# Kernel optimization log

Hardware: AMD Instinct MI355X
Metric: run time of the kernel (lower is better)

Reference implementation:

```python
import jax, jax.numpy as jnp
from jax import lax
import numpy as np

B, T, H, W = 32, 16, 64, 64
LAT, HID, NL = 256, 256, 10
CH = 32  # c_hid
DN = ('NCHW', 'OIHW', 'NCHW')


def setup_inputs() -> dict:
    key = jax.random.key(0)
    keys = iter(jax.random.split(key, 64))
    def rn(shape, scale=0.05):
        return jax.random.normal(next(keys), shape, jnp.float32) * scale
    inp = {}
    inp['x'] = jax.random.normal(next(keys), (B, T, H, W), jnp.float32)
    inp['t'] = jax.random.normal(next(keys), (B, T, H, W), jnp.float32)
    # encoder convs (torch Conv2d weight layout: (out,in,kh,kw))
    inp['ec1_w'] = rn((CH, 1, 3, 3));        inp['ec1_b'] = rn((CH,))
    inp['ec2_w'] = rn((CH, CH, 3, 3));       inp['ec2_b'] = rn((CH,))
    inp['ec3_w'] = rn((2*CH, CH, 3, 3));     inp['ec3_b'] = rn((2*CH,))
    inp['ec4_w'] = rn((2*CH, 2*CH, 3, 3));   inp['ec4_b'] = rn((2*CH,))
    inp['ec5_w'] = rn((2*CH, 2*CH, 3, 3));   inp['ec5_b'] = rn((2*CH,))
    inp['el_w'] = rn((LAT, 2*CH*8*8));       inp['el_b'] = rn((LAT,))
    # decoder (ConvTranspose2d weight layout: (in,out,kh,kw))
    inp['dl_w'] = rn((2*CH*8*8, LAT));       inp['dl_b'] = rn((2*CH*8*8,))
    inp['dt1_w'] = rn((2*CH, 2*CH, 3, 3));   inp['dt1_b'] = rn((2*CH,))
    inp['dc1_w'] = rn((2*CH, 2*CH, 3, 3));   inp['dc1_b'] = rn((2*CH,))
    inp['dt2_w'] = rn((2*CH, CH, 3, 3));     inp['dt2_b'] = rn((CH,))
    inp['dc2_w'] = rn((CH, CH, 3, 3));       inp['dc2_b'] = rn((CH,))
    inp['dt3_w'] = rn((CH, 1, 3, 3));        inp['dt3_b'] = rn((1,))
    # 10 stacked LSTMCells (LAT == HID so layer 0 weight shape matches the rest)
    inp['Wih'] = rn((NL, 4*HID, HID))
    inp['Whh'] = rn((NL, 4*HID, HID))
    inp['bih'] = rn((NL, 4*HID))
    inp['bhh'] = rn((NL, 4*HID))
    inp['lw'] = rn((LAT, HID));  inp['lb'] = rn((LAT,))
    return inp


def gelu(v):
    return jax.nn.gelu(v, approximate=False)


def conv(x, w, b, stride):
    y = lax.conv_general_dilated(x, w, (stride, stride), [(1, 1), (1, 1)], dimension_numbers=DN)
    return y + b[None, :, None, None]


def tconv(x, w, b):
    # torch ConvTranspose2d(k=3, stride=2, padding=1, output_padding=1):
    # flip kernel, swap in/out channels, lhs_dilation=2, pad (lo=1, hi=2)
    wf = jnp.transpose(w[:, :, ::-1, ::-1], (1, 0, 2, 3))
    y = lax.conv_general_dilated(x, wf, (1, 1), [(1, 2), (1, 2)], lhs_dilation=(2, 2), dimension_numbers=DN)
    return y + b[None, :, None, None]


def reference(x, t, ec1_w, ec1_b, ec2_w, ec2_b, ec3_w, ec3_b, ec4_w, ec4_b, ec5_w, ec5_b,
              el_w, el_b, dl_w, dl_b, dt1_w, dt1_b, dc1_w, dc1_b, dt2_w, dt2_b,
              dc2_w, dc2_b, dt3_w, dt3_b, Wih, Whh, bih, bhh, lw, lb):

    def encode(imgs):                              # (N,1,64,64) -> (N,LAT)
        h = gelu(conv(imgs, ec1_w, ec1_b, 2))      # 32x32
        h = gelu(conv(h, ec2_w, ec2_b, 1))
        h = gelu(conv(h, ec3_w, ec3_b, 2))         # 16x16
        h = gelu(conv(h, ec4_w, ec4_b, 1))
        h = gelu(conv(h, ec5_w, ec5_b, 2))         # 8x8
        return h.reshape(h.shape[0], -1) @ el_w.T + el_b

    def decode(z):                                 # (N,LAT) -> (N,1,64,64)
        h = gelu(z @ dl_w.T + dl_b).reshape(z.shape[0], 2*CH, 8, 8)
        h = gelu(tconv(h, dt1_w, dt1_b))           # 16x16
        h = gelu(conv(h, dc1_w, dc1_b, 1))
        h = gelu(tconv(h, dt2_w, dt2_b))           # 32x32
        h = gelu(conv(h, dc2_w, dc2_b, 1))
        return jnp.tanh(tconv(h, dt3_w, dt3_b))    # 64x64

    def cell_stack(h, c, xin):                     # h,c: (NL,B,HID)
        hs, cs = [], []
        prev = xin
        for l in range(NL):
            z = prev @ Wih[l].T + bih[l] + h[l] @ Whh[l].T + bhh[l]
            i, f, g, o = jnp.split(z, 4, axis=-1)
            cl = jax.nn.sigmoid(f) * c[l] + jax.nn.sigmoid(i) * jnp.tanh(g)
            hl = jax.nn.sigmoid(o) * jnp.tanh(cl)
            hs.append(hl); cs.append(cl); prev = hl
        out = prev @ lw.T + lb                     # skip=False
        return jnp.stack(hs), jnp.stack(cs), out

    f_x_t = jnp.concatenate((x, t), axis=1)        # (B,2T,H,W)
    z_x_t = encode(f_x_t.reshape(-1, 1, H, W)).reshape(B, 2 * T, LAT)
    z_x = z_x_t[:, :T]

    h0 = jnp.zeros((NL, B, HID), x.dtype)
    c0 = jnp.zeros((NL, B, HID), x.dtype)

    def step1(carry, xin):
        h, c = carry
        h, c, out = cell_stack(h, c, xin)
        return (h, c), out

    (hT, cT), outs1 = lax.scan(step1, (h0, c0), jnp.swapaxes(z_x, 0, 1))

    def step2(carry, _):
        h, c, xin = carry
        h, c, out = cell_stack(h, c, xin)
        return (h, c, out), out

    _, outs2 = lax.scan(step2, (hT, cT, outs1[-1]), None, length=T)

    outputs = jnp.swapaxes(jnp.concatenate((outs1, outs2), axis=0), 0, 1)  # (B,2T,LAT)
    y_t = outputs[:, T - 1:-1]                    # (B,T,LAT)

    f_t_ = decode(y_t.reshape(B * T, LAT))        # (B*T,1,H,W)
    loss_pred = jnp.mean((f_t_ - f_x_t[:, T:].reshape(-1, 1, H, W)) ** 2)

    f_x_ = decode(z_x.reshape(B * T, LAT))        # rec_loss=True branch
    loss_rec = jnp.mean((f_x_ - f_x_t[:, :T].reshape(-1, 1, H, W)) ** 2)

    return loss_pred, loss_rec, f_t_.reshape(B, T, H, W)
```

## Files before the change

### kernel.cpp

```cpp
#include <hip/hip_runtime.h>
#include <math.h>

#define DEV __device__ __forceinline__

typedef __attribute__((ext_vector_type(8))) short bf8_t;
typedef __attribute__((ext_vector_type(4))) float f4_t;
typedef unsigned short us;

DEV float sigm_f(float v) { return 1.0f / (1.0f + __expf(-v)); }
DEV float tanh_f(float v) { return fmaf(-2.0f, 1.0f / (1.0f + __expf(2.0f * v)), 1.0f); }
DEV float gelu_f(float v) {
  float u = 0.79788456080f * fmaf(0.044715f * v * v, v, v);
  return 0.5f * v * (1.0f + tanh_f(u));
}
DEV unsigned short f2bf(float f) {
  unsigned u = __float_as_uint(f);
  u = (u + 0x7FFFu + ((u >> 16) & 1u)) >> 16;
  return (unsigned short)u;
}
DEV void astore(unsigned* p, unsigned v) {
  __hip_atomic_store(p, v, __ATOMIC_RELAXED, __HIP_MEMORY_SCOPE_AGENT);
}

DEV void prep_norm(int li, const float* w, us* wb, int CIN) {
// ... 22 lines not shown
    const float* __restrict__ dt2, const float* __restrict__ dc2,
    us* __restrict__ o_ec2, us* __restrict__ o_ec3,
    us* __restrict__ o_ec4, us* __restrict__ o_ec5,
    us* __restrict__ o_dt1, us* __restrict__ o_dc1,
    us* __restrict__ o_dt2, us* __restrict__ o_dc2,
    const float* __restrict__ Wih, const float* __restrict__ lw,
    const float* __restrict__ lb,  const float* __restrict__ bih,
    us* __restrict__ wih0b, us* __restrict__ lwTb,
    us* __restrict__ lwbp,  float* __restrict__ beff,
    const float* __restrict__ el_w, const float* __restrict__ dl_w,
    us* __restrict__ elWb, us* __restrict__ dlWb)
{
  int idx = blockIdx.x * 256 + threadIdx.x;
  if (idx < 202752) {
    if (idx < 9216)        prep_norm(idx,          ec2, o_ec2, 32);
    else if (idx < 27648)  prep_norm(idx - 9216,   ec3, o_ec3, 32);
    else if (idx < 64512)  prep_norm(idx - 27648,  ec4, o_ec4, 64);
    else if (idx < 101376) prep_norm(idx - 64512,  ec5, o_ec5, 64);
    else if (idx < 138240) prep_par (idx - 101376, dt1, o_dt1, 64, 64);
    else if (idx < 175104) prep_norm(idx - 138240, dc1, o_dc1, 64);
    else if (idx < 193536) prep_par (idx - 175104, dt2, o_dt2, 32, 64);
    else                   prep_norm(idx - 193536, dc2, o_dc2, 32);
  } else if (idx < 596992) {
    int i2 = idx - 202752;
    if (i2 < 262144) {
      wih0b[i2] = f2bf(Wih[i2]);
    } else if (i2 < 327680) {
      int i = i2 - 262144;
      int n = i & 255, kcol = i >> 8;
      lwTb[i] = f2bf(lw[(size_t)n * 256 + kcol]);
    } else if (i2 < 393216) {
      int i = i2 - 327680;
      lwbp[i] = f2bf(lw[i]);
    } else if (i2 < 394240) {
      int j = i2 - 393216;
      float s = bih[j];
      const float* row = Wih + (size_t)j * 256;
      for (int n = 0; n < 256; ++n) s = fmaf(row[n], lb[n], s);
      beff[j] = s;
    }
  } else {
    int i3 = idx - 596992;
    if (i3 < 1048576) {
      int kn = i3 & 4095, n = i3 >> 12;
      elWb[i3] = f2bf(el_w[(size_t)n * 4096 + ((kn & 63) * 64 + (kn >> 6))]);
    } else {
      int i = i3 - 1048576;
      int k = i & 255, nout = i >> 8;
      dlWb[i] = f2bf(dl_w[(size_t)((nout & 63) * 64 + (nout >> 6)) * 256 + k]);
    }
  }
}

__global__ __launch_bounds__(256) void prep_wl1_k(
    const us* __restrict__ src, us* __restrict__ wb)
{
  int idx = blockIdx.x * 256 + threadIdx.x;
  int e = idx & 7, lane = (idx >> 3) & 63, ks = (idx >> 9) & 7, nt = idx >> 12;
  wb[idx] = src[(size_t)(nt * 16 + (lane & 15)) * 256 + ks * 32 + (lane >> 4) * 8 + e];
}

__global__ __launch_bounds__(256) void ec1_k(
    const float* __restrict__ x,
    const float* __restrict__ w, const float* __restrict__ bias,
    us* __restrict__ out)
{
  __shared__ float sw[288];
  __shared__ float sb[32];
  for (int i = threadIdx.x; i < 288; i += 256) sw[i] = w[i];
  if (threadIdx.x < 32) sb[threadIdx.x] = bias[threadIdx.x];
  __syncthreads();
  int idx = blockIdx.x * 256 + threadIdx.x;
  int ox = idx & 31, oy = (idx >> 5) & 31, n = idx >> 10;
  const float* ip = x + (size_t)n * 4096;
  float pv[9];
#pragma unroll
  for (int kh = 0; kh < 3; ++kh) {
    int iy = oy * 2 + kh - 1;
#pragma unroll
    for (int kw = 0; kw < 3; ++kw) {
      int ix = ox * 2 + kw - 1;
      pv[kh * 3 + kw] = ((unsigned)iy < 64u && (unsigned)ix < 64u) ? ip[iy * 64 + ix] : 0.f;
    }
  }
  us u[32];
#pragma unroll
  for (int co = 0; co < 32; ++co) {
    float a = sb[co];
#pragma unroll
    for (int i = 0; i < 9; ++i) a = fmaf(pv[i], sw[co * 9 + i], a);
    u[co] = f2bf(gelu_f(a));
  }
  us* op = out + (size_t)idx * 32;
#pragma unroll
  for (int p = 0; p < 4; ++p) {
    uint4 v;
    v.x = u[p*8+0] | (u[p*8+1] << 16);
    v.y = u[p*8+2] | (u[p*8+3] << 16);
    v.z = u[p*8+4] | (u[p*8+5] << 16);
    v.w = u[p*8+6] | (u[p*8+7] << 16);
    *(uint4*)&op[p * 8] = v;
  }
}

template<int CIN, int COUT, int HIN, int WIN, int TH, int TW, int MODE>
DEV void convmf_tile(const us* __restrict__ in, const us* __restrict__ wb,
                     const float* __restrict__ bias, us* __restrict__ out,
                     int vb, int nofs, us* lds)
{
  constexpr int HO  = (MODE == 1) ? HIN / 2 : HIN;
  constexpr int WO  = (MODE == 1) ? WIN / 2 : WIN;
  constexpr int TIH = (MODE == 1) ? 2 * TH + 1 : TH + 2;
  constexpr int TIW = (MODE == 1) ? 2 * TW + 1 : TW + 2;
  constexpr int TIWP = (TIW & 1) ? TIW : TIW + 1;
// ... 112 lines not shown
    int4 val = {0, 0, 0, 0};
    if (iy < HIN && ix < WIN)
      val = *(const int4*)&in[(((size_t)n * HIN + iy) * WIN + ix) * CIN + cg * 8];
    *(int4*)&lds[(size_t)((tyy * CG + cg) * TIW + txx) * 8] = val;
  }
  __syncthreads();

  const int lane = threadIdx.x & 63, wv = threadIdx.x >> 6;
  const int l15 = lane & 15, l4 = lane >> 4;
  const int dy = wv >> 1, dx = wv & 1;
  const int NXT = 1 + dx;
  const int KS2 = ((1 + dy) * (1 + dx) * CIN) / 32;
  const int koff = (dy ? (dx ? 5 : 3) : (dx ? 1 : 0)) * CIN;

  f4_t acc[MPW_P][NT] = {};
  for (int ks = 0; ks < KS2; ++ks) {
    const int tapi = (ks * 32) / CIN;
    const int cb = ((ks * 32) % CIN) / 8 + l4;
    const int ra = tapi / NXT, rb = tapi % NXT;
    bf8_t bf[NT];
#pragma unroll
    for (int nt = 0; nt < NT; ++nt)
      bf[nt] = *(const bf8_t*)&wbp[(size_t)(nt * 16 + l15) * 9 * CIN + koff + ks * 32 + 8 * l4];
#pragma unroll
    for (int mi = 0; mi < MPW_P; ++mi) {
      int m = mi * 16 + l15;
      int i = m / SW, j = m % SW;
      bf8_t a = *(const bf8_t*)&lds[(size_t)(((i + ra) * CG + cb) * TIW + (j + rb)) * 8];
#pragma unroll
      for (int nt = 0; nt < NT; ++nt)
        acc[mi][nt] = __builtin_amdgcn_mfma_f32_16x16x32_bf16(a, bf[nt], acc[mi][nt], 0, 0, 0);
    }
  }

#pragma unroll
  for (int mi = 0; mi < MPW_P; ++mi) {
#pragma unroll
    for (int nt = 0; nt < NT; ++nt) {
      int co = nt * 16 + l15;
      float bv = bias[co];
#pragma unroll
      for (int r = 0; r < 4; ++r) {
        int m = mi * 16 + l4 * 4 + r;
        int i = m / SW, j = m % SW;
        int orow = 2 * (ty0s + i) + dy, ocol = 2 * (tx0s + j) + dx;
        float v = acc[mi][nt][r] + bv;
        out[(((size_t)n * HO + orow) * WO + ocol) * COUT + co] = f2bf(gelu_f(v));
      }
    }
  }
  __syncthreads();
}

template<int CIN, int COUT, int HIN, int WIN, int SH, int SW>
__global__ __launch_bounds__(256) void tconvp_k(
    const us* __restrict__ in, const us* __restrict__ wbp,
    const float* __restrict__ bias, us* __restrict__ out)
{
  __shared__ us lds[(SH + 1) * (SW + 1) * (CIN / 8) * 8];
  tconvp_tile<CIN, COUT, HIN, WIN, SH, SW>(in, wbp, bias, out, blockIdx.x, 0, lds);
}

template<int BIASMODE, bool GELU, int OUTMODE>
__global__ __launch_bounds__(256) void gemm16_k(
    const us* __restrict__ A, const us* __restrict__ Bw,
    const float* __restrict__ bias, void* __restrict__ Cv, int M, int N, int K)
{
  const int lane = threadIdx.x & 63, wv = threadIdx.x >> 6;
  const int l15 = lane & 15, l4 = lane >> 4;
  const int mbase = blockIdx.y * 64 + wv * 16;
  const int nbase = blockIdx.x * 64;
  f4_t acc[4] = {};
  for (int k0 = 0; k0 < K; k0 += 32) {
    bf8_t a = *(const bf8_t*)&A[(size_t)(mbase + l15) * K + k0 + 8 * l4];
#pragma unroll
    for (int nt = 0; nt < 4; ++nt) {
      bf8_t b = *(const bf8_t*)&Bw[(size_t)(nbase + nt * 16 + l15) * K + k0 + 8 * l4];
      acc[nt] = __builtin_amdgcn_mfma_f32_16x16x32_bf16(a, b, acc[nt], 0, 0, 0);
    }
  }
#pragma unroll
  for (int nt = 0; nt < 4; ++nt) {
    int col = nbase + nt * 16 + l15;
    float bv = 0.f;
    if (BIASMODE == 0) bv = bias[col];
    if (BIASMODE == 1) bv = bias[(col & 63) * 64 + (col >> 6)];
#pragma unroll
    for (int r = 0; r < 4; ++r) {
      int row = mbase + l4 * 4 + r;
      float v = acc[nt][r] + bv;
      if (GELU) v = gelu_f(v);
      if (OUTMODE == 0)      ((float*)Cv)[(size_t)row * N + col] = v;
      else if (OUTMODE == 1) ((us*)Cv)[(size_t)row * N + col] = f2bf(v);
      else {
        int orow = (row & 31) * 16 + (row >> 5);
        ((us*)Cv)[(size_t)orow * N + col] = f2bf(v);
      }
    }
  }
}

__global__ __launch_bounds__(256) void elgemm_splitk_k(
    const us* __restrict__ A, const us* __restrict__ Bw,
    float* __restrict__ zpart)
{
  const int lane = threadIdx.x & 63, wv = threadIdx.x >> 6;
  const int l15 = lane & 15, l4 = lane >> 4;
  const int mbase = blockIdx.y * 64 + wv * 16;
  const int nbase = blockIdx.x * 64;
  const int kbase = blockIdx.z * 512;
  f4_t acc[4] = {};
  for (int k0 = kbase; k0 < kbase + 512; k0 += 32) {
    bf8_t a = *(const bf8_t*)&A[(size_t)(mbase + l15) * 4096 + k0 + 8 * l4];
#pragma unroll
    for (int nt = 0; nt < 4; ++nt) {
      bf8_t b = *(const bf8_t*)&Bw[(size_t)(nbase + nt * 16 + l15) * 4096 + k0 + 8 * l4];
      acc[nt] = __builtin_amdgcn_mfma_f32_16x16x32_bf16(a, b, acc[nt], 0, 0, 0);
    }
  }
  float* zp = zpart + (size_t)blockIdx.z * 131072;
#pragma unroll
  for (int nt = 0; nt < 4; ++nt) {
    int col = nbase + nt * 16 + l15;
#pragma unroll
    for (int r = 0; r < 4; ++r) {
      int row = mbase + l4 * 4 + r;
      zp[(size_t)row * 256 + col] = acc[nt][r];
    }
  }
}

__global__ __launch_bounds__(256) void zcombine_k(
    const float* __restrict__ zpart, const float* __restrict__ el_b,
    us* __restrict__ zbf, us* __restrict__ ydec)
{
  int idx = blockIdx.x * 256 + threadIdx.x;
  int row = idx >> 8, col = idx & 255;
  float s = el_b[col];
#pragma unroll
  for (int kc = 0; kc < 8; ++kc) s += zpart[(size_t)kc * 131072 + idx];
  int b = row >> 4, tt = row & 15;
  us v = f2bf(s);
  zbf[(size_t)(tt * 32 + b) * 256 + col] = v;
  ydec[(size_t)(512 + row) * 256 + col] = v;
}

DEV void dlgemm_rec_tile(const us* __restrict__ A, const us* __restrict__ Bw,
                         const float* __restrict__ bias, us* __restrict__ C, int vb)
{
  const int lane = threadIdx.x & 63, wv = threadIdx.x >> 6;
  const int l15 = lane & 15, l4 = lane >> 4;
  const int mbase = 512 + (vb >> 6) * 64 + wv * 16;
  const int nbase = (vb & 63) * 64;
  f4_t acc[4] = {};
  for (int k0 = 0; k0 < 256; k0 += 32) {
    bf8_t a = *(const bf8_t*)&A[(size_t)(mbase + l15) * 256 + k0 + 8 * l4];
#pragma unroll
    for (int nt = 0; nt < 4; ++nt) {
      bf8_t b = *(const bf8_t*)&Bw[(size_t)(nbase + nt * 16 + l15) * 256 + k0 + 8 * l4];
      acc[nt] = __builtin_amdgcn_mfma_f32_16x16x32_bf16(a, b, acc[nt], 0, 0, 0);
    }
  }
#pragma unroll
  for (int nt = 0; nt < 4; ++nt) {
    int col = nbase + nt * 16 + l15;
    float bv = bias[(col & 63) * 64 + (col >> 6)];
#pragma unroll
    for (int r = 0; r < 4; ++r) {
      int row = mbase + l4 * 4 + r;
      C[(size_t)row * 4096 + col] = f2bf(gelu_f(acc[nt][r] + bv));
    }
  }
}

DEV void dt3_rec_tile(const us* __restrict__ in, const float* __restrict__ w,
                      const float* __restrict__ bias, const float* __restrict__ xref,
                      float* __restrict__ partials, int vb, float* sw, float* ws4)
{
  for (int i2 = threadIdx.x; i2 < 288; i2 += 256) sw[i2] = w[i2];
  __syncthreads();
  int idx = vb * 256 + threadIdx.x;
  int j = idx & 31, i = (idx >> 5) & 31, nl = idx >> 10;
  int n = 512 + nl;
  bool okj = (j < 31), oki = (i < 31);
  const us* r00 = in + (((size_t)n * 32 + i) * 32 + j) * 32;
  const us* r01 = r00 + 32;
  const us* r10 = r00 + 1024;
  const us* r11 = r10 + 32;
  float b0 = bias[0];
  float acc00 = b0, acc01 = b0, acc10 = b0, acc11 = b0;
  uint4 z4 = {0, 0, 0, 0};
#pragma unroll
  for (int g2 = 0; g2 < 4; ++g2) {
    uint4 v00 = *(const uint4*)&r00[g2 * 8];
    uint4 v01 = okj ? *(const uint4*)&r01[g2 * 8] : z4;
    uint4 v10 = oki ? *(const uint4*)&r10[g2 * 8] : z4;
    uint4 v11 = (oki && okj) ? *(const uint4*)&r11[g2 * 8] : z4;
    unsigned a00[4] = {v00.x, v00.y, v00.z, v00.w};
    unsigned a01[4] = {v01.x, v01.y, v01.z, v01.w};
    unsigned a10[4] = {v10.x, v10.y, v10.z, v10.w};
    unsigned a11[4] = {v11.x, v11.y, v11.z, v11.w};
#pragma unroll
    for (int h2 = 0; h2 < 4; ++h2) {
      int c0 = (g2 * 8 + h2 * 2) * 9;
      float xl, xh;
      xl = __uint_as_float(a00[h2] << 16); xh = __uint_as_float(a00[h2] & 0xffff0000u);
      acc00 = fmaf(xl, sw[c0 + 4], acc00); acc00 = fmaf(xh, sw[c0 + 13], acc00);
      acc01 = fmaf(xl, sw[c0 + 5], acc01); acc01 = fmaf(xh, sw[c0 + 14], acc01);
      acc10 = fmaf(xl, sw[c0 + 7], acc10); acc10 = fmaf(xh, sw[c0 + 16], acc10);
      acc11 = fmaf(xl, sw[c0 + 8], acc11); acc11 = fmaf(xh, sw[c0 + 17], acc11);
      xl = __uint_as_float(a01[h2] << 16); xh = __uint_as_float(a01[h2] & 0xffff0000u);
      acc01 = fmaf(xl, sw[c0 + 3], acc01); acc01 = fmaf(xh, sw[c0 + 12], acc01);
      acc11 = fmaf(xl, sw[c0 + 6], acc11); acc11 = fmaf(xh, sw[c0 + 15], acc11);
      xl = __uint_as_float(a10[h2] << 16); xh = __uint_as_float(a10[h2] & 0xffff0000u);
      acc10 = fmaf(xl, sw[c0 + 1], acc10); acc10 = fmaf(xh, sw[c0 + 10], acc10);
      acc11 = fmaf(xl, sw[c0 + 2], acc11); acc11 = fmaf(xh, sw[c0 + 11], acc11);
      xl = __uint_as_float(a11[h2] << 16); xh = __uint_as_float(a11[h2] & 0xffff0000u);
      acc11 = fmaf(xl, sw[c0 + 0], acc11); acc11 = fmaf(xh, sw[c0 + 9], acc11);
    }
  }
  float o00 = tanh_f(acc00), o01 = tanh_f(acc01);
  float o10 = tanh_f(acc10), o11 = tanh_f(acc11);
  size_t px = (size_t)(2 * i) * 64 + 2 * j;
  const float* xr = xref + (size_t)nl * 4096;
  float d0 = o00 - xr[px],      d1 = o01 - xr[px + 1];
  float d2 = o10 - xr[px + 64], d3 = o11 - xr[px + 65];
  float s = d0 * d0 + d1 * d1 + d2 * d2 + d3 * d3;
#pragma unroll
  for (int off = 32; off > 0; off >>= 1) s += __shfl_down(s, off);
  if ((threadIdx.x & 63) == 0) ws4[threadIdx.x >> 6] = s;
  __syncthreads();
  if (threadIdx.x == 0) partials[2048 + vb] = ws4[0] + ws4[1] + ws4[2] + ws4[3];
  __syncthreads();
}

__global__ __launch_bounds__(256) void dt3_loss_k(
    const us* __restrict__ in, const float* __restrict__ w,
    const float* __restrict__ bias, const float* __restrict__ tref,
    float* __restrict__ fout, float* __restrict__ partials)
{
  __shared__ float sw[288];
  for (int i2 = threadIdx.x; i2 < 288; i2 += 256) sw[i2] = w[i2];
  __syncthreads();
  int idx = blockIdx.x * 256 + threadIdx.x;
  int j = idx & 31, i = (idx >> 5) & 31, n = idx >> 10;
  bool okj = (j < 31), oki = (i < 31);
  const us* r00 = in + (((size_t)n * 32 + i) * 32 + j) * 32;
  const us* r01 = r00 + 32;
  const us* r10 = r00 + 1024;
  const us* r11 = r10 + 32;
  float b0 = bias[0];
  float acc00 = b0, acc01 = b0, acc10 = b0, acc11 = b0;
  uint4 z4 = {0, 0, 0, 0};
#pragma unroll
  for (int g2 = 0; g2 < 4; ++g2) {
    uint4 v00 = *(const uint4*)&r00[g2 * 8];
    uint4 v01 = okj ? *(const uint4*)&r01[g2 * 8] : z4;
    uint4 v10 = oki ? *(const uint4*)&r10[g2 * 8] : z4;
    uint4 v11 = (oki && okj) ? *(const uint4*)&r11[g2 * 8] : z4;
    unsigned a00[4] = {v00.x, v00.y, v00.z, v00.w};
    unsigned a01[4] = {v01.x, v01.y, v01.z, v01.w};
    unsigned a10[4] = {v10.x, v10.y, v10.z, v10.w};
    unsigned a11[4] = {v11.x, v11.y, v11.z, v11.w};
#pragma unroll
    for (int h2 = 0; h2 < 4; ++h2) {
      int c0 = (g2 * 8 + h2 * 2) * 9;
      float xl, xh;
      xl = __uint_as_float(a00[h2] << 16); xh = __uint_as_float(a00[h2] & 0xffff0000u);
      acc00 = fmaf(xl, sw[c0 + 4], acc00); acc00 = fmaf(xh, sw[c0 + 13], acc00);
      acc01 = fmaf(xl, sw[c0 + 5], acc01); acc01 = fmaf(xh, sw[c0 + 14], acc01);
      acc10 = fmaf(xl, sw[c0 + 7], acc10); acc10 = fmaf(xh, sw[c0 + 16], acc10);
      acc11 = fmaf(xl, sw[c0 + 8], acc11); acc11 = fmaf(xh, sw[c0 + 17], acc11);
      xl = __uint_as_float(a01[h2] << 16); xh = __uint_as_float(a01[h2] & 0xffff0000u);
      acc01 = fmaf(xl, sw[c0 + 3], acc01); acc01 = fmaf(xh, sw[c0 + 12], acc01);
      acc11 = fmaf(xl, sw[c0 + 6], acc11); acc11 = fmaf(xh, sw[c0 + 15], acc11);
      xl = __uint_as_float(a10[h2] << 16); xh = __uint_as_float(a10[h2] & 0xffff0000u);
      acc10 = fmaf(xl, sw[c0 + 1], acc10); acc10 = fmaf(xh, sw[c0 + 10], acc10);
      acc11 = fmaf(xl, sw[c0 + 2], acc11); acc11 = fmaf(xh, sw[c0 + 11], acc11);
      xl = __uint_as_float(a11[h2] << 16); xh = __uint_as_float(a11[h2] & 0xffff0000u);
      acc11 = fmaf(xl, sw[c0 + 0], acc11); acc11 = fmaf(xh, sw[c0 + 9], acc11);
    }
  }
  float o00 = tanh_f(acc00), o01 = tanh_f(acc01);
  float o10 = tanh_f(acc10), o11 = tanh_f(acc11);
  size_t px = (size_t)(2 * i) * 64 + 2 * j;
  float* fb = fout + (size_t)n * 4096;
  fb[px] = o00;      fb[px + 1] = o01;
  fb[px + 64] = o10; fb[px + 65] = o11;
  const float* tr = tref + (size_t)n * 4096;
  float d0 = o00 - tr[px],      d1 = o01 - tr[px + 1];
  float d2 = o10 - tr[px + 64], d3 = o11 - tr[px + 65];
  float s = d0 * d0 + d1 * d1 + d2 * d2 + d3 * d3;
#pragma unroll
  for (int off = 32; off > 0; off >>= 1) s += __shfl_down(s, off);
  __shared__ float ws4[4];
  if ((threadIdx.x & 63) == 0) ws4[threadIdx.x >> 6] = s;
  __syncthreads();
  if (threadIdx.x == 0) partials[blockIdx.x] = ws4[0] + ws4[1] + ws4[2] + ws4[3];
}

__global__ __launch_bounds__(256) void loss_final_k(
    const float* __restrict__ partials, float* __restrict__ out01)
{
  __shared__ float red[256];
  int base = blockIdx.x * 2048;
  float s = 0.f;
  for (int i = threadIdx.x; i < 2048; i += 256) s += partials[base + i];
  red[threadIdx.x] = s;
  __syncthreads();
#pragma unroll
  for (int st = 128; st > 0; st >>= 1) {
    if (threadIdx.x < st) red[threadIdx.x] += red[threadIdx.x + st];
    __syncthreads();
  }
  if (threadIdx.x == 0) out01[blockIdx.x] = red[0] * (1.0f / 2097152.0f);
}

#define LSTM_NB 160

DEV void gridbar(unsigned* bar, unsigned target) {
  __syncthreads();
  if (threadIdx.x == 0) {
    __hip_atomic_fetch_add(bar, 1u, __ATOMIC_RELEASE, __HIP_MEMORY_SCOPE_AGENT);
    unsigned spins = 0;
    while (__hip_atomic_load(bar, __ATOMIC_RELAXED, __HIP_MEMORY_SCOPE_AGENT) < target) {
      __builtin_amdgcn_s_sleep(2);
      if (++spins > (1u << 24)) break;
    }
    (void)__hip_atomic_load(bar, __ATOMIC_ACQUIRE, __HIP_MEMORY_SCOPE_AGENT);
  }
  __syncthreads();
}

DEV void spin_min16s(unsigned* f, unsigned tgt) {
  if ((int)tgt <= 0) return;
  unsigned spins = 0;
  for (;;) {
    unsigned m = 0xffffffffu;
#pragma unroll
    for (int i = 0; i < 16; ++i) {
      unsigned v = __hip_atomic_load(f + i * 32, __ATOMIC_RELAXED, __HIP_MEMORY_SCOPE_AGENT);
      m = v < m ? v : m;
    }
    if (m >= tgt) return;
    if (++spins > (1u << 22)) return;
  }
}

__global__ __launch_bounds__(256, 1) void mega_k(
    const float* __restrict__ Wih,
    const float* __restrict__ Whh, const us* __restrict__ meffb,
    const float* __restrict__ bih, const float* __restrict__ bhh,
    const float* __restrict__ beff,
    const us* __restrict__ zbf, us* __restrict__ hbf, us* __restrict__ h9sav,
    unsigned* __restrict__ bar,
    const us* __restrict__ ydec, const us* __restrict__ dlWb,
    const float* __restrict__ dl_b,
    const us* __restrict__ wbp_dt1, const float* __restrict__ dt1_b,
    const us* __restrict__ wb_dc1,  const float* __restrict__ dc1_b,
    const us* __restrict__ wbp_dt2, const float* __restrict__ dt2_b,
    const us* __restrict__ wb_dc2,  const float* __restrict__ dc2_b,
    const float* __restrict__ dt3_w, const float* __restrict__ dt3_b,
    const float* __restrict__ xref,
    us* __restrict__ bufA, us* __restrict__ bufB,
    float* __restrict__ partials)
{
  __shared__ __align__(16) unsigned char smem[109568];

// ... 98 lines not shown
        a0 = __builtin_amdgcn_mfma_f32_16x16x32_bf16(ax0, bwi, a0, 0, 0, 0);
        a1 = __builtin_amdgcn_mfma_f32_16x16x32_bf16(ax1, bwi, a1, 0, 0, 0);
        b0 = __builtin_amdgcn_mfma_f32_16x16x32_bf16(ah0, bwh, b0, 0, 0, 0);
        b1 = __builtin_amdgcn_mfma_f32_16x16x32_bf16(ah1, bwh, b1, 0, 0, 0);
      }
#pragma unroll
      for (int r = 0; r < 4; ++r) {
        zsm[(g * 32 + l4 * 4 + r) * 17 + l15] = a0[r] + b0[r];
        zsm[(g * 32 + 16 + l4 * 4 + r) * 17 + l15] = a1[r] + b1[r];
      }
      __syncthreads();
#pragma unroll
      for (int half = 0; half < 2; ++half) {
        int e = tid + half * 256;
        int b = e >> 4, j = e & 15;
        float zi = zsm[(0 * 32 + b) * 17 + j] + (p2l0 ? sb2[j]      : sbias[j]);
        float zf = zsm[(1 * 32 + b) * 17 + j] + (p2l0 ? sb2[16 + j] : sbias[16 + j]);
        float zg = zsm[(2 * 32 + b) * 17 + j] + (p2l0 ? sb2[32 + j] : sbias[32 + j]);
        float zo = zsm[(3 * 32 + b) * 17 + j] + (p2l0 ? sb2[48 + j] : sbias[48 + j]);
        float cold = cls[b * 16 + j];
        float cn = sigm_f(zf) * cold + sigm_f(zi) * tanh_f(zg);
        cls[b * 16 + j] = cn;
        float hn = sigm_f(zo) * tanh_f(cn);
        float hn_hi = __shfl_down(hn, 1);
        if (!(j & 1)) {
          unsigned pk = (unsigned)f2bf(hn) | ((unsigned)f2bf(hn_hi) << 16);
          astore((unsigned*)&hbf[(size_t)((cur * 10 + l) * 32 + b) * 256 + col0 + j], pk);
          if (l == 9 && t >= 15)
            astore((unsigned*)&h9sav[(size_t)((t - 15) * 32 + b) * 256 + col0 + j], pk);
        }
      }
      __syncthreads();
      if (tid == 0)
        __hip_atomic_store(&fown[jg * 32], (unsigned)(t + 1),
                           __ATOMIC_RELEASE, __HIP_MEMORY_SCOPE_AGENT);
      if (l == 0 && t == 15) {
        for (int c = tid; c < 2048; c += 256) {
          int gg = c >> 9, c2 = c & 511;
          const us* src = meffb + ((size_t)(gg * 16 + jg) * 8) * 512;
          *(int4*)&s_w[(size_t)((gg * 2) * 512 + c2) * 8] = *(const int4*)&src[(size_t)c2 * 8];
        }
        __syncthreads();
      }
    }
  } else {
    us* lds = (us*)smem;
    float* swq = (float*)(smem + 49152);
    float* ws4 = (float*)(smem + 50432);
    unsigned* bar96 = bar + 32;
    const int wg = bid - 160;
    int ep2 = 0;

    for (int vb = wg; vb < 512; vb += 96)
      dlgemm_rec_tile(ydec, dlWb, dl_b, bufB, vb);
    ++ep2; gridbar(bar96, (unsigned)(ep2 * 96));
    for (int vb = wg; vb < 512; vb += 96)
      tconvp_tile<64, 64, 8, 8, 8, 8>(bufB, wbp_dt1, dt1_b, bufA, vb, 512, lds);
    ++ep2; gridbar(bar96, (unsigned)(ep2 * 96));
    for (int vb = wg; vb < 512; vb += 96)
      convmf_tile<64, 64, 16, 16, 16, 16, 0>(bufA, wb_dc1, dc1_b, bufB, vb, 512, lds);
    ++ep2; gridbar(bar96, (unsigned)(ep2 * 96));
    for (int vb = wg; vb < 1024; vb += 96)
      tconvp_tile<64, 32, 16, 16, 8, 16>(bufB, wbp_dt2, dt2_b, bufA, vb, 512, lds);
    ++ep2; gridbar(bar96, (unsigned)(ep2 * 96));
    for (int vb = wg; vb < 2048; vb += 96)
      convmf_tile<32, 32, 32, 32, 16, 16, 0>(bufA, wb_dc2, dc2_b, bufB, vb, 512, lds);
    ++ep2; gridbar(bar96, (unsigned)(ep2 * 96));
    for (int vb = wg; vb < 2048; vb += 96)
      dt3_rec_tile(bufB, dt3_w, dt3_b, xref, partials, vb, swq, ws4);
  }
}

extern "C" void kernel_launch(void* const* d_in, const int* in_sizes, int n_in,
                              void* d_out, int out_size, void* d_ws, size_t ws_size,
                              hipStream_t stream) {
  const float* x     = (const float*)d_in[0];
  const float* t     = (const float*)d_in[1];
  const float* ec1_w = (const float*)d_in[2];
  const float* ec1_b = (const float*)d_in[3];
  const float* ec2_w = (const float*)d_in[4];
  const float* ec2_b = (const float*)d_in[5];
  const float* ec3_w = (const float*)d_in[6];
  const float* ec3_b = (const float*)d_in[7];
  const float* ec4_w = (const float*)d_in[8];
  const float* ec4_b = (const float*)d_in[9];
  const float* ec5_w = (const float*)d_in[10];
  const float* ec5_b = (const float*)d_in[11];
  const float* el_w  = (const float*)d_in[12];
  const float* el_b  = (const float*)d_in[13];
  const float* dl_w  = (const float*)d_in[14];
  const float* dl_b  = (const float*)d_in[15];
  const float* dt1_w = (const float*)d_in[16];
  const float* dt1_b = (const float*)d_in[17];
  const float* dc1_w = (const float*)d_in[18];
  const float* dc1_b = (const float*)d_in[19];
  const float* dt2_w = (const float*)d_in[20];
  const float* dt2_b = (const float*)d_in[21];
  const float* dc2_w = (const float*)d_in[22];
  const float* dc2_b = (const float*)d_in[23];
  const float* dt3_w = (const float*)d_in[24];
  const float* dt3_b = (const float*)d_in[25];
  const float* Wih   = (const float*)d_in[26];
  const float* Whh   = (const float*)d_in[27];
  const float* bih   = (const float*)d_in[28];
  const float* bhh   = (const float*)d_in[29];
  const float* lw    = (const float*)d_in[30];
  const float* lb    = (const float*)d_in[31];
  float* out = (float*)d_out;

  char* base = (char*)d_ws;
  size_t off = 0;
  auto alloc = [&](size_t bytes) -> char* {
    char* p = base + off;
    off += (bytes + 255) & ~(size_t)255;
    return p;
  };
  unsigned* bar   = (unsigned*)alloc(32768);
  float* zpart    = (float*)alloc((size_t)8 * 512 * 256 * 4);
  us*    zbf      = (us*)alloc((size_t)16 * 32 * 256 * 2);
  us*    hbf      = (us*)alloc((size_t)2 * 10 * 32 * 256 * 2);
  us*    h9sav    = (us*)alloc((size_t)16 * 32 * 256 * 2);
  us*    ydec     = (us*)alloc((size_t)1024 * 256 * 2);
  float* partials = (float*)alloc((size_t)16384 * 4);
  us* wb_ec2 = (us*)alloc((size_t)32 * 288 * 2);
  us* wb_ec3 = (us*)alloc((size_t)64 * 288 * 2);
  us* wb_ec4 = (us*)alloc((size_t)64 * 576 * 2);
  us* wb_ec5 = (us*)alloc((size_t)64 * 576 * 2);
  us* wbp_dt1 = (us*)alloc((size_t)64 * 576 * 2);
  us* wb_dc1 = (us*)alloc((size_t)64 * 576 * 2);
  us* wbp_dt2 = (us*)alloc((size_t)32 * 576 * 2);
  us* wb_dc2 = (us*)alloc((size_t)32 * 288 * 2);
  us* elWb   = (us*)alloc((size_t)256 * 4096 * 2);
  us* dlWb   = (us*)alloc((size_t)4096 * 256 * 2);
  us* wih0b  = (us*)alloc((size_t)1024 * 256 * 2);
  us* lwTb   = (us*)alloc((size_t)256 * 256 * 2);
  us* lwbp   = (us*)alloc((size_t)256 * 256 * 2);
  us* meffp  = (us*)alloc((size_t)1024 * 256 * 2);
  us* meffb  = (us*)alloc((size_t)1024 * 256 * 2);
  float* beff = (float*)alloc((size_t)1024 * 4);
  us* enc5   = (us*)alloc((size_t)512 * 4096 * 2);
  us* bufA   = (us*)alloc((size_t)1024 * 32 * 32 * 32 * 2);
  us* bufB   = (us*)alloc((size_t)1024 * 32 * 32 * 32 * 2);
  (void)in_sizes; (void)n_in; (void)out_size; (void)ws_size;

  hipMemsetAsync(bar, 0, 32768, stream);

  prep_all_k<<<10524, 256, 0, stream>>>(ec2_w, ec3_w, ec4_w, ec5_w,
                                        dt1_w, dc1_w, dt2_w, dc2_w,
                                        wb_ec2, wb_ec3, wb_ec4, wb_ec5,
                                        wbp_dt1, wb_dc1, wbp_dt2, wb_dc2,
                                        Wih, lw, lb, bih, wih0b, lwTb, lwbp, beff,
                                        el_w, dl_w, elWb, dlWb);
  gemm16_k<2, false, 1><<<dim3(4, 16), 256, 0, stream>>>(wih0b, lwTb, lb, meffp, 1024, 256, 256);
  prep_wl1_k<<<1024, 256, 0, stream>>>(meffp, meffb);

  ec1_k<<<2048, 256, 0, stream>>>(x, ec1_w, ec1_b, bufA);
  convmf_k<32, 32, 32, 32, 16, 16, 0><<<2048, 256, 0, stream>>>(bufA, wb_ec2, ec2_b, bufB);
  convmf_k<32, 64, 32, 32, 16, 16, 1><<<512, 256, 0, stream>>>(bufB, wb_ec3, ec3_b, bufA);
  convmf_k<64, 64, 16, 16, 16, 16, 0><<<512, 256, 0, stream>>>(bufA, wb_ec4, ec4_b, bufB);
  convmf_k<64, 64, 16, 16, 8, 8, 1><<<512, 256, 0, stream>>>(bufB, wb_ec5, ec5_b, enc5);
  elgemm_splitk_k<<<dim3(4, 8, 8), 256, 0, stream>>>(enc5, elWb, zpart);
  zcombine_k<<<512, 256, 0, stream>>>(zpart, el_b, zbf, ydec);

  mega_k<<<256, 256, 0, stream>>>(Wih, Whh, meffb, bih, bhh, beff,
                                  zbf, hbf, h9sav, bar,
                                  ydec, dlWb, dl_b,
                                  wbp_dt1, dt1_b, wb_dc1, dc1_b,
                                  wbp_dt2, dt2_b, wb_dc2, dc2_b,
                                  dt3_w, dt3_b, x, bufA, bufB, partials);

  gemm16_k<0, false, 2><<<dim3(4, 8), 256, 0, stream>>>(
      h9sav, lwbp, lb, ydec, 512, 256, 256);
  gemm16_k<1, true, 1><<<dim3(64, 8), 256, 0, stream>>>(ydec, dlWb, dl_b, bufB, 1024, 4096, 256);
  tconvp_k<64, 64, 8, 8, 8, 8><<<512, 256, 0, stream>>>(bufB, wbp_dt1, dt1_b, bufA);
  convmf_k<64, 64, 16, 16, 16, 16, 0><<<512, 256, 0, stream>>>(bufA, wb_dc1, dc1_b, bufB);
  tconvp_k<64, 32, 16, 16, 8, 16><<<1024, 256, 0, stream>>>(bufB, wbp_dt2, dt2_b, bufA);
  convmf_k<32, 32, 32, 32, 16, 16, 0><<<2048, 256, 0, stream>>>(bufA, wb_dc2, dc2_b, bufB);
  dt3_loss_k<<<2048, 256, 0, stream>>>(bufB, dt3_w, dt3_b, t, out + 2, partials);
  loss_final_k<<<2, 256, 0, stream>>>(partials, out);
}
```

Before: 1.048 ms.

## Fuse prediction decoder launches into one persistent kernel with grid barriers

Replaces the eight separate prediction-decoder kernel launches (output GEMM, dl GEMM, tconv/conv stages, dt3 loss, final reduction) with a single persistent 768-block kernel. It uses a flag-array software grid barrier between stages. It also folds the prep_wl1 relayout into the meff GEMM epilogue through a new output mode. The goal is to remove launch gaps and tail idle time between small kernels. In exchange, co-residency of all 768 blocks is required, and the per-stage barrier cost and any spin-timeout path add risk.

```diff
diff --git a/kernel.cpp b/kernel.cpp
--- a/kernel.cpp
+++ b/kernel.cpp
@@ -98,14 +98,6 @@
   }
 }
 
-__global__ __launch_bounds__(256) void prep_wl1_k(
-    const us* __restrict__ src, us* __restrict__ wb)
-{
-  int idx = blockIdx.x * 256 + threadIdx.x;
-  int e = idx & 7, lane = (idx >> 3) & 63, ks = (idx >> 9) & 7, nt = idx >> 12;
-  wb[idx] = src[(size_t)(nt * 16 + (lane & 15)) * 256 + ks * 32 + (lane >> 4) * 8 + e];
-}
-
 __global__ __launch_bounds__(256) void ec1_k(
     const float* __restrict__ x,
     const float* __restrict__ w, const float* __restrict__ bias,
@@ -324,15 +316,6 @@
   __syncthreads();
 }
 
-template<int CIN, int COUT, int HIN, int WIN, int SH, int SW>
-__global__ __launch_bounds__(256) void tconvp_k(
-    const us* __restrict__ in, const us* __restrict__ wbp,
-    const float* __restrict__ bias, us* __restrict__ out)
-{
-  __shared__ us lds[(SH + 1) * (SW + 1) * (CIN / 8) * 8];
-  tconvp_tile<CIN, COUT, HIN, WIN, SH, SW>(in, wbp, bias, out, blockIdx.x, 0, lds);
-}
-
 template<int BIASMODE, bool GELU, int OUTMODE>
 __global__ __launch_bounds__(256) void gemm16_k(
     const us* __restrict__ A, const us* __restrict__ Bw,
@@ -364,9 +347,10 @@
       if (GELU) v = gelu_f(v);
       if (OUTMODE == 0)      ((float*)Cv)[(size_t)row * N + col] = v;
       else if (OUTMODE == 1) ((us*)Cv)[(size_t)row * N + col] = f2bf(v);
-      else {
-        int orow = (row & 31) * 16 + (row >> 5);
-        ((us*)Cv)[(size_t)orow * N + col] = f2bf(v);
+      else if (OUTMODE == 3) {
+        int nt2 = row >> 4, l15d = row & 15;
+        int ks2 = col >> 5, l4d = (col >> 3) & 3, e2 = col & 7;
+        ((us*)Cv)[(size_t)nt2 * 4096 + ks2 * 512 + (l4d * 16 + l15d) * 8 + e2] = f2bf(v);
       }
     }
   }
@@ -417,12 +401,42 @@
   ydec[(size_t)(512 + row) * 256 + col] = v;
 }
 
-DEV void dlgemm_rec_tile(const us* __restrict__ A, const us* __restrict__ Bw,
-                         const float* __restrict__ bias, us* __restrict__ C, int vb)
+DEV void outsgemm_tile(const us* __restrict__ A, const us* __restrict__ Bw,
+                       const float* __restrict__ bias, us* __restrict__ ydec, int vb)
 {
   const int lane = threadIdx.x & 63, wv = threadIdx.x >> 6;
   const int l15 = lane & 15, l4 = lane >> 4;
-  const int mbase = 512 + (vb >> 6) * 64 + wv * 16;
+  const int mbase = (vb >> 2) * 64 + wv * 16;
+  const int nbase = (vb & 3) * 64;
+  f4_t acc[4] = {};
+  for (int k0 = 0; k0 < 256; k0 += 32) {
+    bf8_t a = *(const bf8_t*)&A[(size_t)(mbase + l15) * 256 + k0 + 8 * l4];
+#pragma unroll
+    for (int nt = 0; nt < 4; ++nt) {
+      bf8_t b = *(const bf8_t*)&Bw[(size_t)(nbase + nt * 16 + l15) * 256 + k0 + 8 * l4];
+      acc[nt] = __builtin_amdgcn_mfma_f32_16x16x32_bf16(a, b, acc[nt], 0, 0, 0);
+    }
+  }
+#pragma unroll
+  for (int nt = 0; nt < 4; ++nt) {
+    int col = nbase + nt * 16 + l15;
+    float bv = bias[col];
+#pragma unroll
+    for (int r = 0; r < 4; ++r) {
+      int row = mbase + l4 * 4 + r;
+      int orow = (row & 31) * 16 + (row >> 5);
+      ydec[(size_t)orow * 256 + col] = f2bf(acc[nt][r] + bv);
+    }
+  }
+}
+
+DEV void dlgemm_tile(const us* __restrict__ A, const us* __restrict__ Bw,
+                     const float* __restrict__ bias, us* __restrict__ C,
+                     int vb, int rofs)
+{
+  const int lane = threadIdx.x & 63, wv = threadIdx.x >> 6;
+  const int l15 = lane & 15, l4 = lane >> 4;
+  const int mbase = rofs + (vb >> 6) * 64 + wv * 16;
   const int nbase = (vb & 63) * 64;
   f4_t acc[4] = {};
   for (int k0 = 0; k0 < 256; k0 += 32) {
@@ -445,15 +459,17 @@
   }
 }
 
-DEV void dt3_rec_tile(const us* __restrict__ in, const float* __restrict__ w,
-                      const float* __restrict__ bias, const float* __restrict__ xref,
-                      float* __restrict__ partials, int vb, float* sw, float* ws4)
+template<int PRED>
+DEV void dt3_tile(const us* __restrict__ in, const float* __restrict__ w,
+                  const float* __restrict__ bias, const float* __restrict__ ref,
+                  float* __restrict__ fout, float* __restrict__ partials,
+                  int vb, float* sw, float* ws4)
 {
   for (int i2 = threadIdx.x; i2 < 288; i2 += 256) sw[i2] = w[i2];
   __syncthreads();
   int idx = vb * 256 + threadIdx.x;
   int j = idx & 31, i = (idx >> 5) & 31, nl = idx >> 10;
-  int n = 512 + nl;
+  int n = PRED ? nl : (512 + nl);
   bool okj = (j < 31), oki = (i < 31);
   const us* r00 = in + (((size_t)n * 32 + i) * 32 + j) * 32;
   const us* r01 = r00 + 32;
@@ -494,98 +510,21 @@
   float o00 = tanh_f(acc00), o01 = tanh_f(acc01);
   float o10 = tanh_f(acc10), o11 = tanh_f(acc11);
   size_t px = (size_t)(2 * i) * 64 + 2 * j;
-  const float* xr = xref + (size_t)nl * 4096;
-  float d0 = o00 - xr[px],      d1 = o01 - xr[px + 1];
-  float d2 = o10 - xr[px + 64], d3 = o11 - xr[px + 65];
+  if (PRED) {
+    float* fb = fout + (size_t)nl * 4096;
+    fb[px] = o00;      fb[px + 1] = o01;
+    fb[px + 64] = o10; fb[px + 65] = o11;
+  }
+  const float* rr = ref + (size_t)nl * 4096;
+  float d0 = o00 - rr[px],      d1 = o01 - rr[px + 1];
+  float d2 = o10 - rr[px + 64], d3 = o11 - rr[px + 65];
   float s = d0 * d0 + d1 * d1 + d2 * d2 + d3 * d3;
 #pragma unroll
   for (int off = 32; off > 0; off >>= 1) s += __shfl_down(s, off);
   if ((threadIdx.x & 63) == 0) ws4[threadIdx.x >> 6] = s;
   __syncthreads();
-  if (threadIdx.x == 0) partials[2048 + vb] = ws4[0] + ws4[1] + ws4[2] + ws4[3];
-  __syncthreads();
-}
-
-__global__ __launch_bounds__(256) void dt3_loss_k(
-    const us* __restrict__ in, const float* __restrict__ w,
-    const float* __restrict__ bias, const float* __restrict__ tref,
-    float* __restrict__ fout, float* __restrict__ partials)
-{
-  __shared__ float sw[288];
-  for (int i2 = threadIdx.x; i2 < 288; i2 += 256) sw[i2] = w[i2];
-  __syncthreads();
-  int idx = blockIdx.x * 256 + threadIdx.x;
-  int j = idx & 31, i = (idx >> 5) & 31, n = idx >> 10;
-  bool okj = (j < 31), oki = (i < 31);
-  const us* r00 = in + (((size_t)n * 32 + i) * 32 + j) * 32;
-  const us* r01 = r00 + 32;
-  const us* r10 = r00 + 1024;
-  const us* r11 = r10 + 32;
-  float b0 = bias[0];
-  float acc00 = b0, acc01 = b0, acc10 = b0, acc11 = b0;
-  uint4 z4 = {0, 0, 0, 0};
-#pragma unroll
-  for (int g2 = 0; g2 < 4; ++g2) {
-    uint4 v00 = *(const uint4*)&r00[g2 * 8];
-    uint4 v01 = okj ? *(const uint4*)&r01[g2 * 8] : z4;
-    uint4 v10 = oki ? *(const uint4*)&r10[g2 * 8] : z4;
-    uint4 v11 = (oki && okj) ? *(const uint4*)&r11[g2 * 8] : z4;
-    unsigned a00[4] = {v00.x, v00.y, v00.z, v00.w};
-    unsigned a01[4] = {v01.x, v01.y, v01.z, v01.w};
-    unsigned a10[4] = {v10.x, v10.y, v10.z, v10.w};
-    unsigned a11[4] = {v11.x, v11.y, v11.z, v11.w};
-#pragma unroll
-    for (int h2 = 0; h2 < 4; ++h2) {
-      int c0 = (g2 * 8 + h2 * 2) * 9;
-      float xl, xh;
-      xl = __uint_as_float(a00[h2] << 16); xh = __uint_as_float(a00[h2] & 0xffff0000u);
-      acc00 = fmaf(xl, sw[c0 + 4], acc00); acc00 = fmaf(xh, sw[c0 + 13], acc00);
-      acc01 = fmaf(xl, sw[c0 + 5], acc01); acc01 = fmaf(xh, sw[c0 + 14], acc01);
-      acc10 = fmaf(xl, sw[c0 + 7], acc10); acc10 = fmaf(xh, sw[c0 + 16], acc10);
-      acc11 = fmaf(xl, sw[c0 + 8], acc11); acc11 = fmaf(xh, sw[c0 + 17], acc11);
-      xl = __uint_as_float(a01[h2] << 16); xh = __uint_as_float(a01[h2] & 0xffff0000u);
-      acc01 = fmaf(xl, sw[c0 + 3], acc01); acc01 = fmaf(xh, sw[c0 + 12], acc01);
-      acc11 = fmaf(xl, sw[c0 + 6], acc11); acc11 = fmaf(xh, sw[c0 + 15], acc11);
-      xl = __uint_as_float(a10[h2] << 16); xh = __uint_as_float(a10[h2] & 0xffff0000u);
-      acc10 = fmaf(xl, sw[c0 + 1], acc10); acc10 = fmaf(xh, sw[c0 + 10], acc10);
-      acc11 = fmaf(xl, sw[c0 + 2], acc11); acc11 = fmaf(xh, sw[c0 + 11], acc11);
-      xl = __uint_as_float(a11[h2] << 16); xh = __uint_as_float(a11[h2] & 0xffff0000u);
-      acc11 = fmaf(xl, sw[c0 + 0], acc11); acc11 = fmaf(xh, sw[c0 + 9], acc11);
-    }
-  }
-  float o00 = tanh_f(acc00), o01 = tanh_f(acc01);
-  float o10 = tanh_f(acc10), o11 = tanh_f(acc11);
-  size_t px = (size_t)(2 * i) * 64 + 2 * j;
-  float* fb = fout + (size_t)n * 4096;
-  fb[px] = o00;      fb[px + 1] = o01;
-  fb[px + 64] = o10; fb[px + 65] = o11;
-  const float* tr = tref + (size_t)n * 4096;
-  float d0 = o00 - tr[px],      d1 = o01 - tr[px + 1];
-  float d2 = o10 - tr[px + 64], d3 = o11 - tr[px + 65];
-  float s = d0 * d0 + d1 * d1 + d2 * d2 + d3 * d3;
-#pragma unroll
-  for (int off = 32; off > 0; off >>= 1) s += __shfl_down(s, off);
-  __shared__ float ws4[4];
-  if ((threadIdx.x & 63) == 0) ws4[threadIdx.x >> 6] = s;
-  __syncthreads();
-  if (threadIdx.x == 0) partials[blockIdx.x] = ws4[0] + ws4[1] + ws4[2] + ws4[3];
-}
-
-__global__ __launch_bounds__(256) void loss_final_k(
-    const float* __restrict__ partials, float* __restrict__ out01)
-{
-  __shared__ float red[256];
-  int base = blockIdx.x * 2048;
-  float s = 0.f;
-  for (int i = threadIdx.x; i < 2048; i += 256) s += partials[base + i];
-  red[threadIdx.x] = s;
-  __syncthreads();
-#pragma unroll
-  for (int st = 128; st > 0; st >>= 1) {
-    if (threadIdx.x < st) red[threadIdx.x] += red[threadIdx.x + st];
-    __syncthreads();
-  }
-  if (threadIdx.x == 0) out01[blockIdx.x] = red[0] * (1.0f / 2097152.0f);
+  if (threadIdx.x == 0) partials[(PRED ? 0 : 2048) + vb] = ws4[0] + ws4[1] + ws4[2] + ws4[3];
+  __syncthreads();
 }
 
 #define LSTM_NB 160
@@ -790,7 +729,7 @@
     int ep2 = 0;
 
     for (int vb = wg; vb < 512; vb += 96)
-      dlgemm_rec_tile(ydec, dlWb, dl_b, bufB, vb);
+      dlgemm_tile(ydec, dlWb, dl_b, bufB, vb, 512);
     ++ep2; gridbar(bar96, (unsigned)(ep2 * 96));
     for (int vb = wg; vb < 512; vb += 96)
       tconvp_tile<64, 64, 8, 8, 8, 8>(bufB, wbp_dt1, dt1_b, bufA, vb, 512, lds);
@@ -805,7 +744,82 @@
       convmf_tile<32, 32, 32, 32, 16, 16, 0>(bufA, wb_dc2, dc2_b, bufB, vb, 512, lds);
     ++ep2; gridbar(bar96, (unsigned)(ep2 * 96));
     for (int vb = wg; vb < 2048; vb += 96)
-      dt3_rec_tile(bufB, dt3_w, dt3_b, xref, partials, vb, swq, ws4);
+      dt3_tile<0>(bufB, dt3_w, dt3_b, xref, (float*)0, partials, vb, swq, ws4);
+  }
+}
+
+DEV void predbar(unsigned* pf, unsigned ep) {
+  __syncthreads();
+  if (threadIdx.x == 0)
+    __hip_atomic_store(&pf[(size_t)blockIdx.x * 32], ep,
+                       __ATOMIC_RELEASE, __HIP_MEMORY_SCOPE_AGENT);
+  unsigned spins = 0;
+  for (int s = threadIdx.x; s < 768; s += 256) {
+    while (__hip_atomic_load(&pf[(size_t)s * 32],
+                             __ATOMIC_RELAXED, __HIP_MEMORY_SCOPE_AGENT) < ep) {
+      if (++spins > (1u << 25)) break;
+    }
+  }
+  (void)__hip_atomic_load(&pf[(size_t)threadIdx.x * 32],
+                          __ATOMIC_ACQUIRE, __HIP_MEMORY_SCOPE_AGENT);
+  __syncthreads();
+}
+
+__global__ __launch_bounds__(256, 3) void predm_k(
+    const us* __restrict__ h9sav, const us* __restrict__ lwbp,
+    const float* __restrict__ lb,  us* __restrict__ ydec,
+    const us* __restrict__ dlWb,   const float* __restrict__ dl_b,
+    const us* __restrict__ wbp_dt1, const float* __restrict__ dt1_b,
+    const us* __restrict__ wb_dc1,  const float* __restrict__ dc1_b,
+    const us* __restrict__ wbp_dt2, const float* __restrict__ dt2_b,
+    const us* __restrict__ wb_dc2,  const float* __restrict__ dc2_b,
+    const float* __restrict__ dt3_w, const float* __restrict__ dt3_b,
+    const float* __restrict__ tref,
+    us* __restrict__ bufA, us* __restrict__ bufB,
+    float* __restrict__ fout, float* __restrict__ partials,
+    float* __restrict__ out01, unsigned* __restrict__ pf)
+{
+  __shared__ __align__(16) unsigned char smem[45056];
+  us* lds = (us*)smem;
+  float* swq = (float*)(smem + 43776);
+  float* ws4 = (float*)(smem + 44928);
+  const int bid = blockIdx.x;
+  unsigned ep = 0;
+
+  for (int vb = bid; vb < 32; vb += 768)
+    outsgemm_tile(h9sav, lwbp, lb, ydec, vb);
+  ++ep; predbar(pf, ep);
+  for (int vb = bid; vb < 512; vb += 768)
+    dlgemm_tile(ydec, dlWb, dl_b, bufB, vb, 0);
+  ++ep; predbar(pf, ep);
+  for (int vb = bid; vb < 512; vb += 768)
+    tconvp_tile<64, 64, 8, 8, 8, 8>(bufB, wbp_dt1, dt1_b, bufA, vb, 0, lds);
+  ++ep; predbar(pf, ep);
+  for (int vb = bid; vb < 512; vb += 768)
+    convmf_tile<64, 64, 16, 16, 16, 16, 0>(bufA, wb_dc1, dc1_b, bufB, vb, 0, lds);
+  ++ep; predbar(pf, ep);
+  for (int vb = bid; vb < 1024; vb += 768)
+    tconvp_tile<64, 32, 16, 16, 8, 16>(bufB, wbp_dt2, dt2_b, bufA, vb, 0, lds);
+  ++ep; predbar(pf, ep);
+  for (int vb = bid; vb < 2048; vb += 768)
+    convmf_tile<32, 32, 32, 32, 16, 16, 0>(bufA, wb_dc2, dc2_b, bufB, vb, 0, lds);
+  ++ep; predbar(pf, ep);
+  for (int vb = bid; vb < 2048; vb += 768)
+    dt3_tile<1>(bufB, dt3_w, dt3_b, tref, fout, partials, vb, swq, ws4);
+  ++ep; predbar(pf, ep);
+  if (bid < 2) {
+    float* red = (float*)smem;
+    int base = bid * 2048;
+    float s = 0.f;
+    for (int i = threadIdx.x; i < 2048; i += 256) s += partials[base + i];
+    red[threadIdx.x] = s;
+    __syncthreads();
+#pragma unroll
+    for (int st = 128; st > 0; st >>= 1) {
+      if (threadIdx.x < st) red[threadIdx.x] += red[threadIdx.x + st];
+      __syncthreads();
+    }
+    if (threadIdx.x == 0) out01[bid] = red[0] * (1.0f / 2097152.0f);
   }
 }
 
@@ -853,7 +867,7 @@
     off += (bytes + 255) & ~(size_t)255;
     return p;
   };
-  unsigned* bar   = (unsigned*)alloc(32768);
+  unsigned* bar   = (unsigned*)alloc(163840);
   float* zpart    = (float*)alloc((size_t)8 * 512 * 256 * 4);
   us*    zbf      = (us*)alloc((size_t)16 * 32 * 256 * 2);
   us*    hbf      = (us*)alloc((size_t)2 * 10 * 32 * 256 * 2);
@@ -873,7 +887,6 @@
   us* wih0b  = (us*)alloc((size_t)1024 * 256 * 2);
   us* lwTb   = (us*)alloc((size_t)256 * 256 * 2);
   us* lwbp   = (us*)alloc((size_t)256 * 256 * 2);
-  us* meffp  = (us*)alloc((size_t)1024 * 256 * 2);
   us* meffb  = (us*)alloc((size_t)1024 * 256 * 2);
   float* beff = (float*)alloc((size_t)1024 * 4);
   us* enc5   = (us*)alloc((size_t)512 * 4096 * 2);
@@ -881,7 +894,8 @@
   us* bufB   = (us*)alloc((size_t)1024 * 32 * 32 * 32 * 2);
   (void)in_sizes; (void)n_in; (void)out_size; (void)ws_size;
 
-  hipMemsetAsync(bar, 0, 32768, stream);
+  hipMemsetAsync(bar, 0, 163840, stream);
+  unsigned* pf = bar + 8192;
 
   prep_all_k<<<10524, 256, 0, stream>>>(ec2_w, ec3_w, ec4_w, ec5_w,
                                         dt1_w, dc1_w, dt2_w, dc2_w,
@@ -889,8 +903,7 @@
                                         wbp_dt1, wb_dc1, wbp_dt2, wb_dc2,
                                         Wih, lw, lb, bih, wih0b, lwTb, lwbp, beff,
                                         el_w, dl_w, elWb, dlWb);
-  gemm16_k<2, false, 1><<<dim3(4, 16), 256, 0, stream>>>(wih0b, lwTb, lb, meffp, 1024, 256, 256);
-  prep_wl1_k<<<1024, 256, 0, stream>>>(meffp, meffb);
+  gemm16_k<2, false, 3><<<dim3(4, 16), 256, 0, stream>>>(wih0b, lwTb, lb, meffb, 1024, 256, 256);
 
   ec1_k<<<2048, 256, 0, stream>>>(x, ec1_w, ec1_b, bufA);
   convmf_k<32, 32, 32, 32, 16, 16, 0><<<2048, 256, 0, stream>>>(bufA, wb_ec2, ec2_b, bufB);
@@ -907,13 +920,9 @@
                                   wbp_dt2, dt2_b, wb_dc2, dc2_b,
                                   dt3_w, dt3_b, x, bufA, bufB, partials);
 
-  gemm16_k<0, false, 2><<<dim3(4, 8), 256, 0, stream>>>(
-      h9sav, lwbp, lb, ydec, 512, 256, 256);
-  gemm16_k<1, true, 1><<<dim3(64, 8), 256, 0, stream>>>(ydec, dlWb, dl_b, bufB, 1024, 4096, 256);
-  tconvp_k<64, 64, 8, 8, 8, 8><<<512, 256, 0, stream>>>(bufB, wbp_dt1, dt1_b, bufA);
-  convmf_k<64, 64, 16, 16, 16, 16, 0><<<512, 256, 0, stream>>>(bufA, wb_dc1, dc1_b, bufB);
-  tconvp_k<64, 32, 16, 16, 8, 16><<<1024, 256, 0, stream>>>(bufB, wbp_dt2, dt2_b, bufA);
-  convmf_k<32, 32, 32, 32, 16, 16, 0><<<2048, 256, 0, stream>>>(bufA, wb_dc2, dc2_b, bufB);
-  dt3_loss_k<<<2048, 256, 0, stream>>>(bufB, dt3_w, dt3_b, t, out + 2, partials);
-  loss_final_k<<<2, 256, 0, stream>>>(partials, out);
-}
+  predm_k<<<768, 256, 0, stream>>>(h9sav, lwbp, lb, ydec, dlWb, dl_b,
+                                   wbp_dt1, dt1_b, wb_dc1, dc1_b,
+                                   wbp_dt2, dt2_b, wb_dc2, dc2_b,
+                                   dt3_w, dt3_b, t,
+                                   bufA, bufB, out + 2, partials, out, pf);
+}
```

Measured after the change: 1.615 ms. 54.1% more time.
